# Kernel optimization log

Hardware: AMD Instinct MI355X
Metric: run time of the kernel (lower is better)

The kernel has to match this reference:

```python
import jax, jax.numpy as jnp
import numpy as np


def _binarize(x):
    # sign binarize: +1 for x > 0, -1 for x <= 0 (matches torch: ones_like, then -1 where <=0)
    return jnp.where(x <= 0, -1.0, 1.0).astype(x.dtype)


def setup_inputs() -> dict:
    key = jax.random.key(0)
    kx, kw = jax.random.split(key)
    x = jax.random.normal(kx, (32, 256, 56, 56), dtype=jnp.float32)
    weight = jax.random.normal(kw, (256, 256, 3, 3), dtype=jnp.float32) * 0.05
    return {"x": x, "weight": weight}


def reference(x, weight):
    xb = _binarize(x)
    wb = _binarize(weight)
    # NCHW input, OIHW weight; stride 1, padding 1, dilation 1, groups 1
    out = jax.lax.conv_general_dilated(
        xb, wb,
        window_strides=(1, 1),
        padding=((1, 1), (1, 1)),
        rhs_dilation=(1, 1),
        dimension_numbers=("NCHW", "OIHW", "NCHW"),
        feature_group_count=1,
    )
    return out
```

## Files before the change

kernel.cpp:

```cpp
#include <hip/hip_runtime.h>
#include <stdint.h>


#define N_BATCH 32
#define C_IN    256
#define HH      56
#define WW_     56
#define HW      (HH * WW_)
#define C_OUT   256
#define WORDS   8
#define TAPS    9
#define OBLK    8

__global__ __launch_bounds__(256) void pack_x_kernel(const float* __restrict__ x,
                                                     uint32_t* __restrict__ xp) {
    int tid = blockIdx.x * 256 + threadIdx.x;
    int s = tid % HW;
    int t = tid / HW;
    int n = t % N_BATCH;
    int word = t / N_BATCH;
    const float* px = x + ((size_t)(n * C_IN + word * 32)) * HW + s;
    uint32_t bits = 0;
#pragma unroll
    for (int i = 0; i < 32; ++i) {
        float v = px[(size_t)i * HW];
        bits |= (v > 0.0f ? 1u : 0u) << i;
    }
    xp[((size_t)(n * HW + s)) * WORDS + word] = bits;
}

__global__ __launch_bounds__(256) void pack_w_kernel(const float* __restrict__ w,
                                                     uint32_t* __restrict__ wp) {
    int tid = blockIdx.x * 256 + threadIdx.x;
    int o = tid / (TAPS * WORDS);
    int r = tid % (TAPS * WORDS);
    int tap = r / WORDS;
    int j = r % WORDS;
    uint32_t bits = 0;
#pragma unroll
    for (int i = 0; i < 32; ++i) {
        int c = j * 32 + i;
        float v = w[((size_t)(o * C_IN + c)) * TAPS + tap];
        bits |= (v > 0.0f ? 1u : 0u) << i;
    }
    wp[tid] = bits;
}

__global__ __launch_bounds__(256) void bconv_kernel(const uint32_t* __restrict__ xp,
                                                    const uint32_t* __restrict__ wp,
                                                    float* __restrict__ out) {
    int s = blockIdx.x * 256 + threadIdx.x;
    if (s >= HW) return;
    int n = blockIdx.z;
    int o_base = blockIdx.y * OBLK;
    int h = s / WW_;
    int w = s % WW_;

    int acc[OBLK];
#pragma unroll
    for (int o = 0; o < OBLK; ++o) acc[o] = 0;
    int nvalid = 0;

    const uint32_t* xpn = xp + (size_t)n * HW * WORDS;

#pragma unroll
    for (int kh = -1; kh <= 1; ++kh) {
        int hh = h + kh;
        if (hh < 0 || hh >= HH) continue;
#pragma unroll
        for (int kw = -1; kw <= 1; ++kw) {
            int ww = w + kw;
            if (ww < 0 || ww >= WW_) continue;
            ++nvalid;
            const uint32_t* px = xpn + (size_t)(hh * WW_ + ww) * WORDS;
            uint4 a = *reinterpret_cast<const uint4*>(px);
            uint4 b = *reinterpret_cast<const uint4*>(px + 4);
            uint32_t xw[8] = {a.x, a.y, a.z, a.w, b.x, b.y, b.z, b.w};
            int tap = (kh + 1) * 3 + (kw + 1);
#pragma unroll
            for (int o = 0; o < OBLK; ++o) {
                const uint32_t* pw = wp + ((size_t)(o_base + o) * TAPS + tap) * WORDS;
#pragma unroll
                for (int j = 0; j < WORDS; ++j) {
                    acc[o] += __popc(xw[j] ^ pw[j]);
                }
            }
        }
    }

#pragma unroll
    for (int o = 0; o < OBLK; ++o) {
        out[((size_t)(n * C_OUT + o_base + o)) * HW + s] =
            (float)(C_IN * nvalid - 2 * acc[o]);
    }
}

extern "C" void kernel_launch(void* const* d_in, const int* in_sizes, int n_in,
                              void* d_out, int out_size, void* d_ws, size_t ws_size,
                              hipStream_t stream) {
    const float* x = (const float*)d_in[0];
    const float* w = (const float*)d_in[1];
    float* out = (float*)d_out;

    uint32_t* xp = (uint32_t*)d_ws;
    uint32_t* wp = xp + (size_t)N_BATCH * HW * WORDS;

    pack_x_kernel<<<dim3(HW * N_BATCH * WORDS / 256), 256, 0, stream>>>(x, xp);
    pack_w_kernel<<<dim3(C_OUT * TAPS * WORDS / 256), 256, 0, stream>>>(w, wp);

    dim3 grid((HW + 255) / 256, C_OUT / OBLK, N_BATCH);
    bconv_kernel<<<grid, 256, 0, stream>>>(xp, wp, out);
}
```

Before: 278.7 us.

## Zero-pad packed input and correct borders with precomputed weight popcount terms

Packs the binarized input into a spatially zero-padded buffer so the conv inner loop has no boundary branches. Padding bits read as -1, so a small kernel precomputes a per-output-channel correction for each of the nine border classes from the weight popcounts, and the main kernel adds it at the end. This removes divergent control flow in the inner loop. In exchange it adds a memset of the padded buffer, an extra single-block kernel, and a per-thread correction load.

```diff
diff --git a/kernel.cpp b/kernel.cpp
--- a/kernel.cpp
+++ b/kernel.cpp
@@ -11,6 +11,8 @@
 #define WORDS   8
 #define TAPS    9
 #define OBLK    8
+#define PH      58
+#define PW      58
 
 __global__ __launch_bounds__(256) void pack_x_kernel(const float* __restrict__ x,
                                                      uint32_t* __restrict__ xp) {
@@ -19,6 +21,7 @@
     int t = tid / HW;
     int n = t % N_BATCH;
     int word = t / N_BATCH;
+    int h = s / WW_, w = s % WW_;
     const float* px = x + ((size_t)(n * C_IN + word * 32)) * HW + s;
     uint32_t bits = 0;
 #pragma unroll
@@ -26,7 +29,7 @@
         float v = px[(size_t)i * HW];
         bits |= (v > 0.0f ? 1u : 0u) << i;
     }
-    xp[((size_t)(n * HW + s)) * WORDS + word] = bits;
+    xp[(((size_t)n * PH + (h + 1)) * PW + (w + 1)) * WORDS + word] = bits;
 }
 
 __global__ __launch_bounds__(256) void pack_w_kernel(const float* __restrict__ w,
@@ -46,8 +49,41 @@
     wp[tid] = bits;
 }
 
+__global__ void corr_kernel(const uint32_t* __restrict__ wp,
+                            uint32_t* __restrict__ corrT) {
+    int o = threadIdx.x;
+    int pc[TAPS];
+#pragma unroll
+    for (int tap = 0; tap < TAPS; ++tap) {
+        int c = 0;
+#pragma unroll
+        for (int j = 0; j < WORDS; ++j)
+            c += __popc(wp[((size_t)o * TAPS + tap) * WORDS + j]);
+        pc[tap] = c;
+    }
+#pragma unroll
+    for (int hp = 0; hp < 3; ++hp) {
+#pragma unroll
+        for (int wq = 0; wq < 3; ++wq) {
+            int nv = (hp == 1 ? 3 : 2) * (wq == 1 ? 3 : 2);
+            int sinv = 0;
+#pragma unroll
+            for (int kh = -1; kh <= 1; ++kh) {
+#pragma unroll
+                for (int kw = -1; kw <= 1; ++kw) {
+                    bool inv = (kh == -1 && hp == 0) || (kh == 1 && hp == 2) ||
+                               (kw == -1 && wq == 0) || (kw == 1 && wq == 2);
+                    if (inv) sinv += pc[(kh + 1) * 3 + (kw + 1)];
+                }
+            }
+            corrT[(hp * 3 + wq) * C_OUT + o] = (uint32_t)(256 * nv + 2 * sinv);
+        }
+    }
+}
+
 __global__ __launch_bounds__(256) void bconv_kernel(const uint32_t* __restrict__ xp,
                                                     const uint32_t* __restrict__ wp,
+                                                    const uint32_t* __restrict__ corrT,
                                                     float* __restrict__ out) {
     int s = blockIdx.x * 256 + threadIdx.x;
     if (s >= HW) return;
@@ -56,23 +92,17 @@
     int h = s / WW_;
     int w = s % WW_;
 
+    const uint32_t* base = xp + (((size_t)n * PH + (h + 1)) * PW + (w + 1)) * WORDS;
+
     int acc[OBLK];
 #pragma unroll
     for (int o = 0; o < OBLK; ++o) acc[o] = 0;
-    int nvalid = 0;
-
-    const uint32_t* xpn = xp + (size_t)n * HW * WORDS;
 
 #pragma unroll
     for (int kh = -1; kh <= 1; ++kh) {
-        int hh = h + kh;
-        if (hh < 0 || hh >= HH) continue;
 #pragma unroll
         for (int kw = -1; kw <= 1; ++kw) {
-            int ww = w + kw;
-            if (ww < 0 || ww >= WW_) continue;
-            ++nvalid;
-            const uint32_t* px = xpn + (size_t)(hh * WW_ + ww) * WORDS;
+            const uint32_t* px = base + (kh * PW + kw) * WORDS;
             uint4 a = *reinterpret_cast<const uint4*>(px);
             uint4 b = *reinterpret_cast<const uint4*>(px + 4);
             uint32_t xw[8] = {a.x, a.y, a.z, a.w, b.x, b.y, b.z, b.w};
@@ -88,10 +118,14 @@
         }
     }
 
+    int hp = (h == 0) ? 0 : ((h == HH - 1) ? 2 : 1);
+    int wq = (w == 0) ? 0 : ((w == WW_ - 1) ? 2 : 1);
+    const uint32_t* ct = corrT + (hp * 3 + wq) * C_OUT + o_base;
+
 #pragma unroll
     for (int o = 0; o < OBLK; ++o) {
         out[((size_t)(n * C_OUT + o_base + o)) * HW + s] =
-            (float)(C_IN * nvalid - 2 * acc[o]);
+            (float)((int)ct[o] - 2 * acc[o]);
     }
 }
 
@@ -102,12 +136,16 @@
     const float* w = (const float*)d_in[1];
     float* out = (float*)d_out;
 
-    uint32_t* xp = (uint32_t*)d_ws;
-    uint32_t* wp = xp + (size_t)N_BATCH * HW * WORDS;
+    uint32_t* xp    = (uint32_t*)d_ws;
+    uint32_t* wp    = xp + (size_t)N_BATCH * PH * PW * WORDS;
+    uint32_t* corrT = wp + (size_t)C_OUT * TAPS * WORDS;
+
+    hipMemsetAsync(xp, 0, (size_t)N_BATCH * PH * PW * WORDS * sizeof(uint32_t), stream);
 
     pack_x_kernel<<<dim3(HW * N_BATCH * WORDS / 256), 256, 0, stream>>>(x, xp);
     pack_w_kernel<<<dim3(C_OUT * TAPS * WORDS / 256), 256, 0, stream>>>(w, wp);
+    corr_kernel<<<dim3(1), 256, 0, stream>>>(wp, corrT);
 
     dim3 grid((HW + 255) / 256, C_OUT / OBLK, N_BATCH);
-    bconv_kernel<<<grid, 256, 0, stream>>>(xp, wp, out);
+    bconv_kernel<<<grid, 256, 0, stream>>>(xp, wp, corrT, out);
 }
```

After: 292.9 us. 1.05x slower.

## Replace XNOR-popcount convolution with int8 MFMA implicit GEMM over padded input

Applied to the files above, without the earlier changes.

The per-pixel XOR/popcount loop is replaced by an implicit GEMM on int8 MFMA (32x32x32). Input sign bits are packed into a zero-halo padded layout. Bits are expanded on the fly to +1/-1 bytes, with halo pixels mapped to 0. Weights are pre-expanded to signed bytes in a swizzled order. Tiles are double-buffered in LDS with XOR swizzling to avoid bank conflicts, moving the work onto matrix cores at the cost of more LDS traffic and expansion ALU work.

```diff
diff --git a/kernel.cpp b/kernel.cpp
--- a/kernel.cpp
+++ b/kernel.cpp
@@ -2,97 +2,190 @@
 #include <stdint.h>
 
 
+typedef int i32x4 __attribute__((ext_vector_type(4)));
+typedef int i32x16 __attribute__((ext_vector_type(16)));
+typedef unsigned int u32;
+
 #define N_BATCH 32
-#define C_IN    256
-#define HH      56
-#define WW_     56
-#define HW      (HH * WW_)
-#define C_OUT   256
-#define WORDS   8
-#define TAPS    9
-#define OBLK    8
-
-__global__ __launch_bounds__(256) void pack_x_kernel(const float* __restrict__ x,
-                                                     uint32_t* __restrict__ xp) {
-    int tid = blockIdx.x * 256 + threadIdx.x;
-    int s = tid % HW;
-    int t = tid / HW;
-    int n = t % N_BATCH;
-    int word = t / N_BATCH;
-    const float* px = x + ((size_t)(n * C_IN + word * 32)) * HW + s;
-    uint32_t bits = 0;
-#pragma unroll
-    for (int i = 0; i < 32; ++i) {
-        float v = px[(size_t)i * HW];
-        bits |= (v > 0.0f ? 1u : 0u) << i;
+#define C_IN 256
+#define C_OUT 256
+#define HH 56
+#define WW_ 56
+#define HW 3136
+#define PH 58
+#define PW 58
+#define WORDS 8
+#define KD 576
+
+static __device__ __forceinline__ u32 expand4(u32 srcw, int sh, u32 tbl) {
+    u32 u = (srcw >> sh) & 0xFu;
+    u32 sp = u;
+    sp |= u << 7;
+    sp |= u << 14;
+    sp |= u << 21;
+    sp &= 0x01010101u;
+#if __has_builtin(__builtin_amdgcn_perm)
+    return __builtin_amdgcn_perm(0u, tbl, sp);
+#else
+    u32 r = 0;
+#pragma unroll
+    for (int i = 0; i < 4; ++i) {
+        u32 bit = (sp >> (8 * i)) & 1u;
+        u32 b = (tbl == 0u) ? 0u : (bit ? 0x01u : 0xFFu);
+        r |= b << (8 * i);
     }
-    xp[((size_t)(n * HW + s)) * WORDS + word] = bits;
-}
-
-__global__ __launch_bounds__(256) void pack_w_kernel(const float* __restrict__ w,
-                                                     uint32_t* __restrict__ wp) {
-    int tid = blockIdx.x * 256 + threadIdx.x;
-    int o = tid / (TAPS * WORDS);
-    int r = tid % (TAPS * WORDS);
-    int tap = r / WORDS;
-    int j = r % WORDS;
-    uint32_t bits = 0;
-#pragma unroll
-    for (int i = 0; i < 32; ++i) {
-        int c = j * 32 + i;
-        float v = w[((size_t)(o * C_IN + c)) * TAPS + tap];
-        bits |= (v > 0.0f ? 1u : 0u) << i;
+    return r;
+#endif
+}
+
+__global__ __launch_bounds__(256) void prep_x(const float* __restrict__ x,
+                                              u32* __restrict__ xp) {
+    int sx = blockIdx.x * 64 + threadIdx.x;
+    int word = blockIdx.y * 4 + threadIdx.y;
+    int n = blockIdx.z;
+    int h = sx / 56, w2 = sx - h * 56;
+    const float* px = x + ((size_t)(n * C_IN + word * 32)) * HW + sx;
+    u32 bits = 0;
+#pragma unroll
+    for (int i = 0; i < 32; ++i)
+        bits |= (px[(size_t)i * HW] > 0.0f ? 1u : 0u) << i;
+    xp[(((size_t)n * PH + (h + 1)) * PW + (w2 + 1)) * WORDS + word] = bits;
+}
+
+__global__ __launch_bounds__(256) void prep_w(const float* __restrict__ wt,
+                                              u32* __restrict__ wq) {
+    int d = blockIdx.x * 256 + threadIdx.x;
+    int o = d / KD;
+    int kq = d - o * KD;
+    int k = kq * 4;
+    int tap = k >> 8;
+    int c = k & 255;
+    const float* ws = wt + ((size_t)o * C_IN + c) * 9 + tap;
+    u32 r = 0;
+#pragma unroll
+    for (int i = 0; i < 4; ++i) {
+        u32 b = (ws[(size_t)i * 9] > 0.0f) ? 0x01u : 0xFFu;
+        r |= b << (8 * i);
     }
-    wp[tid] = bits;
-}
-
-__global__ __launch_bounds__(256) void bconv_kernel(const uint32_t* __restrict__ xp,
-                                                    const uint32_t* __restrict__ wp,
-                                                    float* __restrict__ out) {
-    int s = blockIdx.x * 256 + threadIdx.x;
-    if (s >= HW) return;
-    int n = blockIdx.z;
-    int o_base = blockIdx.y * OBLK;
-    int h = s / WW_;
-    int w = s % WW_;
-
-    int acc[OBLK];
-#pragma unroll
-    for (int o = 0; o < OBLK; ++o) acc[o] = 0;
-    int nvalid = 0;
-
-    const uint32_t* xpn = xp + (size_t)n * HW * WORDS;
-
-#pragma unroll
-    for (int kh = -1; kh <= 1; ++kh) {
-        int hh = h + kh;
-        if (hh < 0 || hh >= HH) continue;
-#pragma unroll
-        for (int kw = -1; kw <= 1; ++kw) {
-            int ww = w + kw;
-            if (ww < 0 || ww >= WW_) continue;
-            ++nvalid;
-            const uint32_t* px = xpn + (size_t)(hh * WW_ + ww) * WORDS;
-            uint4 a = *reinterpret_cast<const uint4*>(px);
-            uint4 b = *reinterpret_cast<const uint4*>(px + 4);
-            uint32_t xw[8] = {a.x, a.y, a.z, a.w, b.x, b.y, b.z, b.w};
-            int tap = (kh + 1) * 3 + (kw + 1);
-#pragma unroll
-            for (int o = 0; o < OBLK; ++o) {
-                const uint32_t* pw = wp + ((size_t)(o_base + o) * TAPS + tap) * WORDS;
-#pragma unroll
-                for (int j = 0; j < WORDS; ++j) {
-                    acc[o] += __popc(xw[j] ^ pw[j]);
-                }
-            }
+    int chunk = (k >> 4) & 7;
+    int pchunk = chunk ^ (o & 7);
+    int gk = (k & ~127) | (pchunk << 4) | (k & 15);
+    wq[(size_t)o * KD + (gk >> 2)] = r;
+}
+
+__global__ __launch_bounds__(256, 2) void bgemm(const u32* __restrict__ xp,
+                                                const u32* __restrict__ wq,
+                                                float* __restrict__ out) {
+    __shared__ __align__(16) u32 Wl[2][128 * 32];
+    __shared__ __align__(16) u32 Xl[2][128 * 32];
+
+    const int tid = threadIdx.x;
+    const int l = tid & 63;
+    const int wave = tid >> 6;
+    const int wm = wave >> 1, wn = wave & 1;
+    const int la = l & 31, lg = l >> 5;
+
+    const int pxb = blockIdx.x;
+    const int ob = blockIdx.y;
+    const int n = blockIdx.z;
+
+    const int px_l = tid >> 1;
+    const int hf = tid & 1;
+    int px_g = pxb * 128 + px_l;
+    if (px_g > HW - 1) px_g = HW - 1;
+    const int ih = px_g / 56;
+    const int iw = px_g - ih * 56;
+
+    const int wc = tid & 7;
+    const int wo0 = (tid >> 3) << 2;
+    const u32* wbase = wq + ((size_t)(ob * 128 + wo0)) * KD + wc * 4;
+
+    i32x16 acc00 = {0}, acc01 = {0}, acc10 = {0}, acc11 = {0};
+
+    const int rowA0 = wm * 64 + la;
+    const int rowB0 = wn * 64 + la;
+
+    u32 xd0, xd1, xtbl;
+    i32x4 wv0, wv1, wv2, wv3;
+
+    auto LOAD = [&](int kc) {
+        int tap = kc >> 1, cc = kc & 1;
+        int rr = tap / 3, tt = tap - rr * 3;
+        int hp = ih + rr, wp2 = iw + tt;
+        bool halo = (hp == 0) | (hp == PH - 1) | (wp2 == 0) | (wp2 == PW - 1);
+        const u32* src = xp + (((size_t)n * PH + hp) * PW + wp2) * WORDS + cc * 4 + hf * 2;
+        xd0 = src[0];
+        xd1 = src[1];
+        xtbl = halo ? 0u : 0x000001FFu;
+        const u32* ws = wbase + (size_t)kc * 32;
+        wv0 = *(const i32x4*)(ws);
+        wv1 = *(const i32x4*)(ws + KD);
+        wv2 = *(const i32x4*)(ws + 2 * KD);
+        wv3 = *(const i32x4*)(ws + 3 * KD);
+    };
+
+    auto WRITE = [&](int buf) {
+        u32 outd[16];
+#pragma unroll
+        for (int q = 0; q < 16; ++q)
+            outd[q] = expand4((q < 8) ? xd0 : xd1, (q & 7) * 4, xtbl);
+#pragma unroll
+        for (int w = 0; w < 4; ++w) {
+            int phys = ((hf * 4 + w) ^ (px_l & 7)) * 4;
+            *(i32x4*)&Xl[buf][px_l * 32 + phys] = *(const i32x4*)&outd[w * 4];
         }
+        *(i32x4*)&Wl[buf][(wo0 + 0) * 32 + wc * 4] = wv0;
+        *(i32x4*)&Wl[buf][(wo0 + 1) * 32 + wc * 4] = wv1;
+        *(i32x4*)&Wl[buf][(wo0 + 2) * 32 + wc * 4] = wv2;
+        *(i32x4*)&Wl[buf][(wo0 + 3) * 32 + wc * 4] = wv3;
+    };
+
+    auto COMPUTE = [&](int buf) {
+#pragma unroll
+        for (int kk = 0; kk < 4; ++kk) {
+            int phys = (((kk * 2 + lg) ^ (la & 7)) << 2);
+            i32x4 a0 = *(const i32x4*)&Wl[buf][(rowA0)      * 32 + phys];
+            i32x4 a1 = *(const i32x4*)&Wl[buf][(rowA0 + 32) * 32 + phys];
+            i32x4 b0 = *(const i32x4*)&Xl[buf][(rowB0)      * 32 + phys];
+            i32x4 b1 = *(const i32x4*)&Xl[buf][(rowB0 + 32) * 32 + phys];
+            acc00 = __builtin_amdgcn_mfma_i32_32x32x32_i8(a0, b0, acc00, 0, 0, 0);
+            acc01 = __builtin_amdgcn_mfma_i32_32x32x32_i8(a0, b1, acc01, 0, 0, 0);
+            acc10 = __builtin_amdgcn_mfma_i32_32x32x32_i8(a1, b0, acc10, 0, 0, 0);
+            acc11 = __builtin_amdgcn_mfma_i32_32x32x32_i8(a1, b1, acc11, 0, 0, 0);
+        }
+    };
+
+    LOAD(0);
+    WRITE(0);
+    __syncthreads();
+
+    int cur = 0;
+#pragma unroll 1
+    for (int kc = 0; kc < 18; ++kc) {
+        if (kc < 17) LOAD(kc + 1);
+        COMPUTE(cur);
+        if (kc < 17) WRITE(cur ^ 1);
+        __syncthreads();
+        cur ^= 1;
     }
 
-#pragma unroll
-    for (int o = 0; o < OBLK; ++o) {
-        out[((size_t)(n * C_OUT + o_base + o)) * HW + s] =
-            (float)(C_IN * nvalid - 2 * acc[o]);
-    }
+    const int og0 = ob * 128 + wm * 64;
+    const int pxg0 = pxb * 128 + wn * 64;
+    float* outn = out + (size_t)n * C_OUT * HW;
+
+    auto STORE = [&](const i32x16& a, int obase, int pbase) {
+        if (pbase >= HW) return;
+        int px = pbase + la;
+#pragma unroll
+        for (int r = 0; r < 16; ++r) {
+            int orow = obase + (r & 3) + 8 * (r >> 2) + 4 * lg;
+            outn[(size_t)orow * HW + px] = (float)a[r];
+        }
+    };
+    STORE(acc00, og0,      pxg0);
+    STORE(acc01, og0,      pxg0 + 32);
+    STORE(acc10, og0 + 32, pxg0);
+    STORE(acc11, og0 + 32, pxg0 + 32);
 }
 
 extern "C" void kernel_launch(void* const* d_in, const int* in_sizes, int n_in,
@@ -102,12 +195,10 @@
     const float* w = (const float*)d_in[1];
     float* out = (float*)d_out;
 
-    uint32_t* xp = (uint32_t*)d_ws;
-    uint32_t* wp = xp + (size_t)N_BATCH * HW * WORDS;
-
-    pack_x_kernel<<<dim3(HW * N_BATCH * WORDS / 256), 256, 0, stream>>>(x, xp);
-    pack_w_kernel<<<dim3(C_OUT * TAPS * WORDS / 256), 256, 0, stream>>>(w, wp);
-
-    dim3 grid((HW + 255) / 256, C_OUT / OBLK, N_BATCH);
-    bconv_kernel<<<grid, 256, 0, stream>>>(xp, wp, out);
-}
+    u32* xp = (u32*)d_ws;
+    u32* wq = xp + (size_t)N_BATCH * PH * PW * WORDS;
+
+    prep_x<<<dim3(49, 2, 32), dim3(64, 4), 0, stream>>>(x, xp);
+    prep_w<<<dim3(576), dim3(256), 0, stream>>>(w, wq);
+    bgemm<<<dim3(25, 2, 32), dim3(256), 0, stream>>>(xp, wq, out);
+}
```

New measurement: 254.2 us. -8.8%, faster.
